# Optimization experiments

Measured on AMD Instinct MI355X. Metric: run time of the kernel, lower is better.

Reference implementation:

```python
import jax, jax.numpy as jnp
import numpy as np
import math

OUT_H, OUT_W = 608 // 4, 1088 // 4   # 152, 272
HW = OUT_H * OUT_W                   # 41344
MAX_OBJS = 256
N_ANN = 64
NID = 537
EMB_DIM = 256
EMB_SCALE = math.sqrt(2.0) * math.log(NID - 1.0)
B = 8


def gaussian_radius(height, width, min_overlap=0.7):
    # standard CenterNet radius; height/width are jnp.ceil'd box sizes
    b1 = height + width
    c1 = width * height * (1.0 - min_overlap) / (1.0 + min_overlap)
    r1 = (b1 + jnp.sqrt(jnp.maximum(b1 * b1 - 4.0 * c1, 0.0))) / 2.0
    b2 = 2.0 * (height + width)
    c2 = (1.0 - min_overlap) * width * height
    r2 = (b2 + jnp.sqrt(jnp.maximum(b2 * b2 - 16.0 * c2, 0.0))) / 2.0
    b3 = -2.0 * min_overlap * (height + width)
    c3 = (min_overlap - 1.0) * width * height
    r3 = (b3 + jnp.sqrt(jnp.maximum(b3 * b3 - 16.0 * min_overlap * c3, 0.0))) / 2.0
    return jnp.minimum(jnp.minimum(r1, r2), r3)


def build_targets(ann1, ann2):
    # ann cols: [cx, cy, w, h, cls, pid, vis, extra]; boxes normalized to [0,1]
    cx_raw = ann1[:, 0] * OUT_W
    cy_raw = ann1[:, 1] * OUT_H
    w = ann1[:, 2] * OUT_W
    h = ann1[:, 3] * OUT_H
    # amodal box from UNclipped center (torch deepcopies before clipping)
    x1 = cx_raw - 0.5 * w; y1 = cy_raw - 0.5 * h
    x2 = x1 + w;           y2 = y1 + h
    cx = jnp.clip(cx_raw, 0.0, OUT_W - 1.0)
    cy = jnp.clip(cy_raw, 0.0, OUT_H - 1.0)
    ctx = cx.astype(jnp.int32)
    cty = cy.astype(jnp.int32)
    radius = jnp.maximum(jnp.floor(gaussian_radius(jnp.ceil(h), jnp.ceil(w))), 0.0)

    # batched gaussian splat, max-reduced over objects (draw_umich_gaussian)
    sigma = (2.0 * radius + 1.0) / 6.0
    dx = jnp.arange(OUT_W, dtype=jnp.float32)[None, :] - ctx[:, None].astype(jnp.float32)  # [N,W]
    dy = jnp.arange(OUT_H, dtype=jnp.float32)[None, :] - cty[:, None].astype(jnp.float32)  # [N,H]
    g = jnp.exp(-(dy[:, :, None] ** 2 + dx[:, None, :] ** 2) / (2.0 * sigma[:, None, None] ** 2))  # [N,H,W]
    win = (jnp.abs(dy)[:, :, None] <= radius[:, None, None]) & (jnp.abs(dx)[:, None, :] <= radius[:, None, None])
    hm = jnp.max(jnp.where(win, g, 0.0), axis=0)  # [H,W]

    # first match of each object's pid in the next frame (torch breaks at first hit)
    pid1 = ann1[:, 5]
    match = pid1[:, None] == ann2[None, :, 5]
    has = match.any(axis=1)
    t1 = ann2[jnp.argmax(match, axis=1)]
    cx2 = t1[:, 0] * OUT_W; cy2 = t1[:, 1] * OUT_H
    w2 = t1[:, 2] * OUT_W;  h2 = t1[:, 3] * OUT_H
    x1t = cx2 - 0.5 * w2; y1t = cy2 - 0.5 * h2
    x2t = x1t + w2;       y2t = y1t + h2

    valid = has & (h > 0) & (w > 0) & (h2 > 0) & (w2 > 0)
    vm = valid.astype(jnp.float32)
    cxf = ctx.astype(jnp.float32); cyf = cty.astype(jnp.float32)
    wh = jnp.stack([cxf - x1, x2 - cxf, cyf - y1, y2 - cyf,
                    cxf - x1t, x2t - cxf, cyf - y1t, y2t - cyf], axis=-1) * vm[:, None]
    ind = jnp.where(valid, cty * OUT_W + ctx, 0)
    v = ann1[:, 6] * vm
    ids = jnp.where(valid, pid1.astype(jnp.int32), 0)

    pad = MAX_OBJS - N_ANN
    return (hm,
            jnp.pad(ind, (0, pad)),
            jnp.pad(vm, (0, pad)),
            jnp.pad(wh, ((0, pad), (0, 0))),
            jnp.pad(v, (0, pad)),
            jnp.pad(ids, (0, pad)))


def focal_loss(pred, gt):
    # CenterNet focal loss; pred already sigmoid+clamped
    pos = (gt == 1.0).astype(pred.dtype)
    pos_loss = (jnp.log(pred) * (1.0 - pred) ** 2 * pos).sum()
    neg_loss = (jnp.log(1.0 - pred) * pred ** 2 * (1.0 - gt) ** 4 * (1.0 - pos)).sum()
    num_pos = pos.sum()
    return jnp.where(num_pos > 0, -(pos_loss + neg_loss) / jnp.maximum(num_pos, 1.0), -neg_loss)


def reg_loss(feat, mask, ind, target):
    # feat [C,HW]; gather per-object channels, masked smooth-L1 sum / num_valid
    pred = feat[:, ind].T                       # [max_objs, C]
    m = mask[:, None]
    d = jnp.abs(pred * m - target * m)
    sl1 = jnp.where(d < 1.0, 0.5 * d * d, d - 0.5)
    return sl1.sum() / (mask.sum() + 1e-4)


def id_loss(identi, ind, mask, v, ids, W_id, b_id):
    feat = identi[:, ind].T                     # [max_objs, 256]
    feat = EMB_SCALE * feat / jnp.maximum(jnp.linalg.norm(feat, axis=-1, keepdims=True), 1e-12)
    logits = feat @ W_id.T + b_id               # [max_objs, 537]
    logp = jax.nn.log_softmax(logits, axis=-1)
    nll = -v * jnp.take_along_axis(logp, ids[:, None], axis=1)[:, 0]
    return (nll * mask).sum() / jnp.maximum(mask.sum(), 1.0)


def reference(classifications, regressions, viss, identis, annotations1, annotations2, W_id, b_id, s_det, s_id):
    cls = jnp.clip(jax.nn.sigmoid(classifications), 1e-4, 1.0 - 1e-4)   # [B,1,HW]
    vis = jnp.clip(jax.nn.sigmoid(viss), 1e-4, 1.0 - 1e-4)              # [B,1,HW]
    hm, ind, mask, wh, v, ids = jax.vmap(build_targets)(annotations1, annotations2)
    cls_l = jax.vmap(lambda p, g: focal_loss(p.reshape(OUT_H, OUT_W), g))(cls, hm)
    reg_l = jax.vmap(reg_loss)(regressions, mask, ind, wh)
    vis_l = jax.vmap(lambda f, m, i, t: reg_loss(f, m, i, t[:, None]))(vis, mask, ind, v)
    id_l = jax.vmap(lambda f, i, m, vv, ii: id_loss(f, i, m, vv, ii, W_id, b_id))(identis, ind, mask, v, ids)
    return (cls_l.mean(keepdims=True), reg_l.mean(keepdims=True), vis_l.mean(keepdims=True),
            id_l.mean(keepdims=True), s_det, s_id)


def setup_inputs() -> dict:
    key = jax.random.key(0)
    ks = jax.random.split(key, 8)
    classifications = jax.random.normal(ks[0], (B, 1, HW), dtype=jnp.float32)
    regressions = jax.random.normal(ks[1], (B, 8, HW), dtype=jnp.float32)
    viss = jax.random.normal(ks[2], (B, 1, HW), dtype=jnp.float32)
    identis = jax.random.normal(ks[3], (B, EMB_DIM, HW), dtype=jnp.float32)

    def make_frame_pair(k):
        k1, k2, k3, k4, k5, k6, k7 = jax.random.split(k, 7)
        cx = jax.random.uniform(k1, (N_ANN,), minval=0.05, maxval=0.95)
        cy = jax.random.uniform(k2, (N_ANN,), minval=0.05, maxval=0.95)
        w = jax.random.uniform(k3, (N_ANN,), minval=0.02, maxval=0.25)
        h = jax.random.uniform(k4, (N_ANN,), minval=0.05, maxval=0.4)
        pid = jax.random.permutation(k5, NID)[:N_ANN].astype(jnp.float32)  # unique track ids
        vis = jax.random.uniform(k6, (N_ANN,))
        extra = jax.random.uniform(k7, (N_ANN,))
        cls = jnp.zeros((N_ANN,), dtype=jnp.float32)
        a1 = jnp.stack([cx, cy, w, h, cls, pid, vis, extra], axis=-1)
        kp, kj = jax.random.split(jax.random.fold_in(k, 99))
        a2 = a1[jax.random.permutation(kp, N_ANN)]
        a2 = a2.at[:, 0:2].add(0.01 * jax.random.normal(kj, (N_ANN, 2)))
        a2 = a2.at[:, 0:2].set(jnp.clip(a2[:, 0:2], 0.05, 0.95))
        return a1, a2

    pairs = [make_frame_pair(jax.random.fold_in(ks[4], b)) for b in range(B)]
    annotations1 = jnp.stack([p[0] for p in pairs])
    annotations2 = jnp.stack([p[1] for p in pairs])
    W_id = 0.02 * jax.random.normal(ks[5], (NID, EMB_DIM), dtype=jnp.float32)
    b_id = jnp.zeros((NID,), dtype=jnp.float32)
    s_det = jnp.array([-1.85], dtype=jnp.float32)
    s_id = jnp.array([-1.05], dtype=jnp.float32)
    return {"classifications": classifications, "regressions": regressions, "viss": viss,
            "identis": identis, "annotations1": annotations1, "annotations2": annotations2,
            "W_id": W_id, "b_id": b_id, "s_det": s_det, "s_id": s_id}
```

## Files before the change

kernel.cpp:

```cpp
#include <hip/hip_runtime.h>
#include <math.h>

#define OUT_H 152
#define OUT_W 272
#define HW 41344
#define NOBJ 64
#define NB 8
#define NID 537
#define EMB 256

#define NFBLK 162
#define NFOCAL (NFBLK * NB)
#define NIDBLK (NB * NOBJ)

#define OF_FP    0
#define OF_IDNLL (NFOCAL * 3)

__device__ inline float waveRedSum(float v) {
  for (int off = 32; off; off >>= 1) v += __shfl_down(v, off, 64);
  return v;
}
__device__ inline float waveRedMax(float v) {
  for (int off = 32; off; off >>= 1) v = fmaxf(v, __shfl_down(v, off, 64));
  return v;
}

struct PrepOut {
  float cxf, cyf, radius, inv2s2, vm, v;
  float wh[8];
  int ind, id;
};

__device__ __forceinline__ PrepOut prep_obj(const float* __restrict__ ann1,
                                            const float* __restrict__ ann2,
                                            int b, int i) {
  const float* a1 = ann1 + (b * NOBJ + i) * 8;
  const float* A2 = ann2 + b * NOBJ * 8;

  float cx_raw = a1[0] * (float)OUT_W;
  float cy_raw = a1[1] * (float)OUT_H;
  float w = a1[2] * (float)OUT_W;
  float h = a1[3] * (float)OUT_H;
  float x1 = cx_raw - 0.5f * w, y1 = cy_raw - 0.5f * h;
  float x2 = x1 + w, y2 = y1 + h;
  float cx = fminf(fmaxf(cx_raw, 0.f), (float)(OUT_W - 1));
  float cy = fminf(fmaxf(cy_raw, 0.f), (float)(OUT_H - 1));
  int ctx = (int)cx, cty = (int)cy;

  float hc = ceilf(h), wc = ceilf(w);
  float b1 = hc + wc;
  float c1 = wc * hc * 0.3f / 1.7f;
  float r1 = (b1 + sqrtf(fmaxf(b1 * b1 - 4.f * c1, 0.f))) * 0.5f;
  float b2 = 2.f * (hc + wc);
  float c2 = 0.3f * wc * hc;
  float r2 = (b2 + sqrtf(fmaxf(b2 * b2 - 16.f * c2, 0.f))) * 0.5f;
  float b3 = -1.4f * (hc + wc);
  float c3 = -0.3f * wc * hc;
  float r3 = (b3 + sqrtf(fmaxf(b3 * b3 - 11.2f * c3, 0.f))) * 0.5f;
  float radius = fmaxf(floorf(fminf(fminf(r1, r2), r3)), 0.f);
  float sigma = (2.f * radius + 1.f) / 6.f;

  PrepOut P;
  P.cxf = (float)ctx;
  P.cyf = (float)cty;
  P.radius = radius;
  P.inv2s2 = 1.f / (2.f * sigma * sigma);

  float pid = a1[5];
  int jm = -1;
  for (int j = 0; j < NOBJ; ++j) {
    if (A2[j * 8 + 5] == pid) { jm = j; break; }
  }
  bool has = (jm >= 0);
  const float* t1 = A2 + (has ? jm : 0) * 8;
  float cx2 = t1[0] * (float)OUT_W, cy2 = t1[1] * (float)OUT_H;
  float w2 = t1[2] * (float)OUT_W, h2 = t1[3] * (float)OUT_H;
  float x1t = cx2 - 0.5f * w2, y1t = cy2 - 0.5f * h2;
  float x2t = x1t + w2, y2t = y1t + h2;

  bool valid = has && (h > 0.f) && (w > 0.f) && (h2 > 0.f) && (w2 > 0.f);
  float vm = valid ? 1.f : 0.f;
  P.vm = vm;
  P.v = a1[6] * vm;
  P.wh[0] = (P.cxf - x1) * vm;  P.wh[1] = (x2 - P.cxf) * vm;
  P.wh[2] = (P.cyf - y1) * vm;  P.wh[3] = (y2 - P.cyf) * vm;
  P.wh[4] = (P.cxf - x1t) * vm; P.wh[5] = (x2t - P.cxf) * vm;
  P.wh[6] = (P.cyf - y1t) * vm; P.wh[7] = (y2t - P.cyf) * vm;
  P.ind = valid ? (cty * OUT_W + ctx) : 0;
  P.id = valid ? (int)pid : 0;
  return P;
}

__global__ void __launch_bounds__(256)
main_kernel(const float* __restrict__ cls,
            const float* __restrict__ identis,
            const float* __restrict__ W_id,
            const float* __restrict__ b_id,
            const float* __restrict__ ann1,
            const float* __restrict__ ann2,
            float* __restrict__ F) {
  if (blockIdx.x < NFOCAL) {
    int blk = blockIdx.x;
    int b = blk / NFBLK;
    int bx = blk - b * NFBLK;
    int p = bx * 256 + threadIdx.x;

    __shared__ float s_ctx[64], s_cty[64], s_rad[64], s_inv[64];
    if (threadIdx.x < 64) {
      PrepOut P = prep_obj(ann1, ann2, b, threadIdx.x);
      s_ctx[threadIdx.x] = P.cxf;
      s_cty[threadIdx.x] = P.cyf;
      s_rad[threadIdx.x] = P.radius;
      s_inv[threadIdx.x] = P.inv2s2;
    }
    __syncthreads();

    float pos_l = 0.f, neg_l = 0.f, npos = 0.f;
    if (p < HW) {
      float xf = (float)(p % OUT_W);
      float yf = (float)(p / OUT_W);
      float gt = 0.f;
      #pragma unroll 8
      for (int o = 0; o < 64; ++o) {
        float dy = yf - s_cty[o];
        float dx = xf - s_ctx[o];
        float r = s_rad[o];
        if (fabsf(dy) <= r && fabsf(dx) <= r) {
          gt = fmaxf(gt, expf(-(dy * dy + dx * dx) * s_inv[o]));
        }
      }
      float x = cls[b * HW + p];
      float pr = 1.f / (1.f + expf(-x));
      pr = fminf(fmaxf(pr, 1e-4f), 0.9999f);
      if (gt == 1.f) {
        float om = 1.f - pr;
        pos_l = logf(pr) * om * om;
        npos = 1.f;
      } else {
        float omg = 1.f - gt;
        float w4 = omg * omg;
        w4 *= w4;
        neg_l = logf(1.f - pr) * pr * pr * w4;
      }
    }

    __shared__ float red[3][4];
    int wid = threadIdx.x >> 6, lane = threadIdx.x & 63;
    float a = waveRedSum(pos_l);
    float c = waveRedSum(neg_l);
    float n = waveRedSum(npos);
    if (lane == 0) { red[0][wid] = a; red[1][wid] = c; red[2][wid] = n; }
    __syncthreads();
    if (threadIdx.x == 0) {
      float pa = 0.f, pc = 0.f, pn = 0.f;
      for (int k = 0; k < 4; ++k) { pa += red[0][k]; pc += red[1][k]; pn += red[2][k]; }
      F[OF_FP + blk * 3 + 0] = pa;
      F[OF_FP + blk * 3 + 1] = pc;
      F[OF_FP + blk * 3 + 2] = pn;
    }
  } else {
    int o = blockIdx.x - NFOCAL;
    int b = o >> 6, i = o & 63;
    PrepOut P = prep_obj(ann1, ann2, b, i);
    if (P.vm == 0.f) {
      if (threadIdx.x == 0) F[OF_IDNLL + o] = 0.f;
      return;
    }
    int t = threadIdx.x;
    __shared__ float shf[EMB];
    __shared__ float slog[544];
    __shared__ float red4[4];
    int wid = t >> 6, lane = t & 63;

    float f = identis[(size_t)b * EMB * HW + (size_t)t * HW + P.ind];
    float n2 = waveRedSum(f * f);
    if (lane == 0) red4[wid] = n2;
    __syncthreads();
    float norm2 = red4[0] + red4[1] + red4[2] + red4[3];
    const float EMB_SCALE = 1.41421356237309515f * logf(536.0f);
    float scale = EMB_SCALE / fmaxf(sqrtf(norm2), 1e-12f);
    shf[t] = f * scale;
    __syncthreads();

    for (int c = t; c < NID; c += 256) {
      float acc = b_id[c];
      const float* wr = W_id + (size_t)c * EMB;
      #pragma unroll 4
      for (int k = 0; k < EMB; k += 4) {
        acc += shf[k] * wr[k] + shf[k + 1] * wr[k + 1] +
               shf[k + 2] * wr[k + 2] + shf[k + 3] * wr[k + 3];
      }
      slog[c] = acc;
    }
    __syncthreads();

    float mx = -1e30f;
    for (int c = t; c < NID; c += 256) mx = fmaxf(mx, slog[c]);
    mx = waveRedMax(mx);
    __syncthreads();
    if (lane == 0) red4[wid] = mx;
    __syncthreads();
    mx = fmaxf(fmaxf(red4[0], red4[1]), fmaxf(red4[2], red4[3]));

    float se = 0.f;
    for (int c = t; c < NID; c += 256) se += expf(slog[c] - mx);
    se = waveRedSum(se);
    __syncthreads();
    if (lane == 0) red4[wid] = se;
    __syncthreads();

    if (t == 0) {
      float sesum = red4[0] + red4[1] + red4[2] + red4[3];
      float lse = mx + logf(sesum);
      F[OF_IDNLL + o] = -P.v * (slog[P.id] - lse);
    }
  }
}

__global__ void __launch_bounds__(512)
final_kernel(const float* __restrict__ reg,
             const float* __restrict__ viss,
             const float* __restrict__ ann1,
             const float* __restrict__ ann2,
             const float* __restrict__ F,
             const float* __restrict__ s_det,
             const float* __restrict__ s_id,
             float* __restrict__ out) {
  int t = threadIdx.x;
  int b = t >> 6;
  int lane = t & 63;

  PrepOut P = prep_obj(ann1, ann2, b, lane);
  float msum = waveRedSum(P.vm);

  float rsum = 0.f, vsum = 0.f;
  if (P.vm > 0.f) {
    for (int c = 0; c < 8; ++c) {
      float pred = reg[(b * 8 + c) * HW + P.ind];
      float d = fabsf(pred - P.wh[c]);
      rsum += (d < 1.f) ? 0.5f * d * d : d - 0.5f;
    }
    float s = 1.f / (1.f + expf(-viss[b * HW + P.ind]));
    s = fminf(fmaxf(s, 1e-4f), 0.9999f);
    float d = fabsf(s - P.v);
    vsum += (d < 1.f) ? 0.5f * d * d : d - 0.5f;
  }
  rsum = waveRedSum(rsum);
  vsum = waveRedSum(vsum);

  float pa = 0.f, pc = 0.f, pn = 0.f;
  for (int e = lane; e < NFBLK; e += 64) {
    const float* fp = F + OF_FP + (b * NFBLK + e) * 3;
    pa += fp[0]; pc += fp[1]; pn += fp[2];
  }
  pa = waveRedSum(pa);
  pc = waveRedSum(pc);
  pn = waveRedSum(pn);

  float idv = waveRedSum(F[OF_IDNLL + b * 64 + lane]);

  __shared__ float L[8][4];
  if (lane == 0) {
    L[b][0] = (pn > 0.f) ? (-(pa + pc) / fmaxf(pn, 1.f)) : (-pc);
    L[b][1] = rsum / (msum + 0.0001f);
    L[b][2] = vsum / (msum + 0.0001f);
    L[b][3] = idv / fmaxf(msum, 1.f);
  }
  __syncthreads();
  if (t == 0) {
    float cl = 0.f, rl = 0.f, vl = 0.f, il = 0.f;
    for (int k = 0; k < 8; ++k) {
      cl += L[k][0]; rl += L[k][1]; vl += L[k][2]; il += L[k][3];
    }
    out[0] = cl / 8.f;
    out[1] = rl / 8.f;
    out[2] = vl / 8.f;
    out[3] = il / 8.f;
    out[4] = s_det[0];
    out[5] = s_id[0];
  }
}

extern "C" void kernel_launch(void* const* d_in, const int* in_sizes, int n_in,
                              void* d_out, int out_size, void* d_ws, size_t ws_size,
                              hipStream_t stream) {
  const float* cls     = (const float*)d_in[0];
  const float* reg     = (const float*)d_in[1];
  const float* viss    = (const float*)d_in[2];
  const float* identis = (const float*)d_in[3];
  const float* ann1    = (const float*)d_in[4];
  const float* ann2    = (const float*)d_in[5];
  const float* W_id    = (const float*)d_in[6];
  const float* b_id    = (const float*)d_in[7];
  const float* s_det   = (const float*)d_in[8];
  const float* s_id    = (const float*)d_in[9];
  float* F = (float*)d_ws;

  main_kernel<<<NFOCAL + NIDBLK, 256, 0, stream>>>(cls, identis, W_id, b_id,
                                                   ann1, ann2, F);
  final_kernel<<<1, 512, 0, stream>>>(reg, viss, ann1, ann2, F,
                                      s_det, s_id, (float*)d_out);
}
```

Before: 60.58 us.

## Move reg/vis loss into ID blocks and use wave-cooperative coalesced logits GEMV

The per-object regression and visibility smooth-L1 terms move out of the single-block final kernel into the per-object ID blocks. They are written as partial sums to the workspace, so the serial tail kernel only reduces precomputed values. The ID logits loop changes from one thread per class reading a whole weight row with strided access to one wave per group of four rows. Each lane loads a float4 of the row, and the partial dot products are combined with shuffle reductions, giving coalesced weight reads. The cost is more shuffle work and lane-0-only stores of the logits.

```diff
diff --git a/kernel.cpp b/kernel.cpp
--- a/kernel.cpp
+++ b/kernel.cpp
@@ -15,6 +15,9 @@
 
 #define OF_FP    0
 #define OF_IDNLL (NFOCAL * 3)
+#define OF_REGP  (OF_IDNLL + 512)
+#define OF_VISP  (OF_REGP + 512)
+#define OF_VMV   (OF_VISP + 512)
 
 __device__ inline float waveRedSum(float v) {
   for (int off = 32; off; off >>= 1) v += __shfl_down(v, off, 64);
@@ -93,6 +96,8 @@
 
 __global__ void __launch_bounds__(256)
 main_kernel(const float* __restrict__ cls,
+            const float* __restrict__ reg,
+            const float* __restrict__ viss,
             const float* __restrict__ identis,
             const float* __restrict__ W_id,
             const float* __restrict__ b_id,
@@ -161,16 +166,39 @@
   } else {
     int o = blockIdx.x - NFOCAL;
     int b = o >> 6, i = o & 63;
+    int t = threadIdx.x;
+    int wid = t >> 6, lane = t & 63;
     PrepOut P = prep_obj(ann1, ann2, b, i);
+
+    if (wid == 0) {
+      float rv = 0.f, vv = 0.f;
+      if (lane < 8) {
+        float pred = reg[(b * 8 + lane) * HW + P.ind];
+        float d = fabsf(pred * P.vm - P.wh[lane]);
+        rv = (d < 1.f) ? 0.5f * d * d : d - 0.5f;
+      } else if (lane == 8) {
+        float s = 1.f / (1.f + expf(-viss[b * HW + P.ind]));
+        s = fminf(fmaxf(s, 1e-4f), 0.9999f);
+        float d = fabsf(s * P.vm - P.v);
+        vv = (d < 1.f) ? 0.5f * d * d : d - 0.5f;
+      }
+      rv = waveRedSum(rv);
+      vv = waveRedSum(vv);
+      if (lane == 0) {
+        F[OF_REGP + o] = rv;
+        F[OF_VISP + o] = vv;
+        F[OF_VMV + o]  = P.vm;
+      }
+    }
+
     if (P.vm == 0.f) {
-      if (threadIdx.x == 0) F[OF_IDNLL + o] = 0.f;
+      if (t == 0) F[OF_IDNLL + o] = 0.f;
       return;
     }
-    int t = threadIdx.x;
+
     __shared__ float shf[EMB];
     __shared__ float slog[544];
     __shared__ float red4[4];
-    int wid = t >> 6, lane = t & 63;
 
     float f = identis[(size_t)b * EMB * HW + (size_t)t * HW + P.ind];
     float n2 = waveRedSum(f * f);
@@ -182,15 +210,30 @@
     shf[t] = f * scale;
     __syncthreads();
 
-    for (int c = t; c < NID; c += 256) {
-      float acc = b_id[c];
-      const float* wr = W_id + (size_t)c * EMB;
-      #pragma unroll 4
-      for (int k = 0; k < EMB; k += 4) {
-        acc += shf[k] * wr[k] + shf[k + 1] * wr[k + 1] +
-               shf[k + 2] * wr[k + 2] + shf[k + 3] * wr[k + 3];
-      }
-      slog[c] = acc;
+    float4 s4 = *(const float4*)&shf[lane * 4];
+    for (int r0 = wid * 4; r0 < NID; r0 += 16) {
+      float acc[4];
+      #pragma unroll
+      for (int rr = 0; rr < 4; ++rr) {
+        int r = r0 + rr;
+        float ax = 0.f;
+        if (r < NID) {
+          const float4 wv = *(const float4*)&W_id[(size_t)r * EMB + lane * 4];
+          ax = wv.x * s4.x + wv.y * s4.y + wv.z * s4.z + wv.w * s4.w;
+        }
+        acc[rr] = ax;
+      }
+      #pragma unroll
+      for (int rr = 0; rr < 4; ++rr)
+        for (int off = 32; off; off >>= 1)
+          acc[rr] += __shfl_down(acc[rr], off, 64);
+      if (lane == 0) {
+        #pragma unroll
+        for (int rr = 0; rr < 4; ++rr) {
+          int r = r0 + rr;
+          if (r < NID) slog[r] = acc[rr] + b_id[r];
+        }
+      }
     }
     __syncthreads();
 
@@ -218,11 +261,7 @@
 }
 
 __global__ void __launch_bounds__(512)
-final_kernel(const float* __restrict__ reg,
-             const float* __restrict__ viss,
-             const float* __restrict__ ann1,
-             const float* __restrict__ ann2,
-             const float* __restrict__ F,
+final_kernel(const float* __restrict__ F,
              const float* __restrict__ s_det,
              const float* __restrict__ s_id,
              float* __restrict__ out) {
@@ -230,24 +269,6 @@
   int b = t >> 6;
   int lane = t & 63;
 
-  PrepOut P = prep_obj(ann1, ann2, b, lane);
-  float msum = waveRedSum(P.vm);
-
-  float rsum = 0.f, vsum = 0.f;
-  if (P.vm > 0.f) {
-    for (int c = 0; c < 8; ++c) {
-      float pred = reg[(b * 8 + c) * HW + P.ind];
-      float d = fabsf(pred - P.wh[c]);
-      rsum += (d < 1.f) ? 0.5f * d * d : d - 0.5f;
-    }
-    float s = 1.f / (1.f + expf(-viss[b * HW + P.ind]));
-    s = fminf(fmaxf(s, 1e-4f), 0.9999f);
-    float d = fabsf(s - P.v);
-    vsum += (d < 1.f) ? 0.5f * d * d : d - 0.5f;
-  }
-  rsum = waveRedSum(rsum);
-  vsum = waveRedSum(vsum);
-
   float pa = 0.f, pc = 0.f, pn = 0.f;
   for (int e = lane; e < NFBLK; e += 64) {
     const float* fp = F + OF_FP + (b * NFBLK + e) * 3;
@@ -257,7 +278,10 @@
   pc = waveRedSum(pc);
   pn = waveRedSum(pn);
 
-  float idv = waveRedSum(F[OF_IDNLL + b * 64 + lane]);
+  float rsum = waveRedSum(F[OF_REGP + b * 64 + lane]);
+  float vsum = waveRedSum(F[OF_VISP + b * 64 + lane]);
+  float msum = waveRedSum(F[OF_VMV  + b * 64 + lane]);
+  float idv  = waveRedSum(F[OF_IDNLL + b * 64 + lane]);
 
   __shared__ float L[8][4];
   if (lane == 0) {
@@ -296,8 +320,7 @@
   const float* s_id    = (const float*)d_in[9];
   float* F = (float*)d_ws;
 
-  main_kernel<<<NFOCAL + NIDBLK, 256, 0, stream>>>(cls, identis, W_id, b_id,
-                                                   ann1, ann2, F);
-  final_kernel<<<1, 512, 0, stream>>>(reg, viss, ann1, ann2, F,
-                                      s_det, s_id, (float*)d_out);
-}
+  main_kernel<<<NFOCAL + NIDBLK, 256, 0, stream>>>(cls, reg, viss, identis,
+                                                   W_id, b_id, ann1, ann2, F);
+  final_kernel<<<1, 512, 0, stream>>>(F, s_det, s_id, (float*)d_out);
+}
```

New measurement: 69.48 us. 1.15x slower.

## Cull gaussian objects per block via ballot mask, use fast math, vectorize ID GEMV

Applied to the files above, without the earlier changes.

Each focal block now computes a 64-bit ballot mask of the objects whose gaussian window overlaps the block's pixel rows or columns, and iterates only over those objects. Object centers and radii are packed into one integer per object. Precise exp and log are replaced with __expf and __logf throughout, and the ID-classifier dot product uses float4 loads. This cuts per-pixel loop work and transcendental cost, at the price of slightly lower math precision and a dependence on the integer bit-packing ranges.

```diff
diff --git a/kernel.cpp b/kernel.cpp
--- a/kernel.cpp
+++ b/kernel.cpp
@@ -103,15 +103,26 @@
     int blk = blockIdx.x;
     int b = blk / NFBLK;
     int bx = blk - b * NFBLK;
-    int p = bx * 256 + threadIdx.x;
-
-    __shared__ float s_ctx[64], s_cty[64], s_rad[64], s_inv[64];
+    int p0 = bx * 256;
+    int p = p0 + threadIdx.x;
+
+    __shared__ unsigned s_pk[64];
+    __shared__ float s_inv[64];
+    __shared__ unsigned long long s_mask;
     if (threadIdx.x < 64) {
       PrepOut P = prep_obj(ann1, ann2, b, threadIdx.x);
-      s_ctx[threadIdx.x] = P.cxf;
-      s_cty[threadIdx.x] = P.cyf;
-      s_rad[threadIdx.x] = P.radius;
+      int ctx = (int)P.cxf, cty = (int)P.cyf, r = (int)P.radius;
+      s_pk[threadIdx.x]  = (unsigned)ctx | ((unsigned)cty << 9) | ((unsigned)r << 17);
       s_inv[threadIdx.x] = P.inv2s2;
+      int y0 = p0 / OUT_W;
+      int y1 = (p0 + 255) / OUT_W;
+      bool two_rows = (y1 > y0);
+      int x0 = two_rows ? 0 : (p0 - y0 * OUT_W);
+      int x1 = two_rows ? (OUT_W - 1) : (p0 + 255 - y0 * OUT_W);
+      bool act = (cty + r >= y0) && (cty - r <= y1) &&
+                 (ctx + r >= x0) && (ctx - r <= x1);
+      unsigned long long m = __ballot(act);
+      if (threadIdx.x == 0) s_mask = m;
     }
     __syncthreads();
 
@@ -120,27 +131,33 @@
       float xf = (float)(p % OUT_W);
       float yf = (float)(p / OUT_W);
       float gt = 0.f;
-      #pragma unroll 8
-      for (int o = 0; o < 64; ++o) {
-        float dy = yf - s_cty[o];
-        float dx = xf - s_ctx[o];
-        float r = s_rad[o];
-        if (fabsf(dy) <= r && fabsf(dx) <= r) {
-          gt = fmaxf(gt, expf(-(dy * dy + dx * dx) * s_inv[o]));
+      unsigned long long m = s_mask;
+      while (m) {
+        int o = __ffsll((unsigned long long)m) - 1;
+        m &= m - 1;
+        unsigned pk = s_pk[o];
+        float inv = s_inv[o];
+        float cxv = (float)(pk & 511u);
+        float cyv = (float)((pk >> 9) & 255u);
+        float rv  = (float)(pk >> 17);
+        float dy = yf - cyv;
+        float dx = xf - cxv;
+        if (fabsf(dy) <= rv && fabsf(dx) <= rv) {
+          gt = fmaxf(gt, __expf(-(dy * dy + dx * dx) * inv));
         }
       }
       float x = cls[b * HW + p];
-      float pr = 1.f / (1.f + expf(-x));
+      float pr = 1.f / (1.f + __expf(-x));
       pr = fminf(fmaxf(pr, 1e-4f), 0.9999f);
       if (gt == 1.f) {
         float om = 1.f - pr;
-        pos_l = logf(pr) * om * om;
+        pos_l = __logf(pr) * om * om;
         npos = 1.f;
       } else {
         float omg = 1.f - gt;
         float w4 = omg * omg;
         w4 *= w4;
-        neg_l = logf(1.f - pr) * pr * pr * w4;
+        neg_l = __logf(1.f - pr) * pr * pr * w4;
       }
     }
 
@@ -185,10 +202,11 @@
     for (int c = t; c < NID; c += 256) {
       float acc = b_id[c];
       const float* wr = W_id + (size_t)c * EMB;
-      #pragma unroll 4
+      #pragma unroll 8
       for (int k = 0; k < EMB; k += 4) {
-        acc += shf[k] * wr[k] + shf[k + 1] * wr[k + 1] +
-               shf[k + 2] * wr[k + 2] + shf[k + 3] * wr[k + 3];
+        float4 wv = *(const float4*)(wr + k);
+        float4 sv = *(const float4*)(&shf[k]);
+        acc += wv.x * sv.x + wv.y * sv.y + wv.z * sv.z + wv.w * sv.w;
       }
       slog[c] = acc;
     }
@@ -203,7 +221,7 @@
     mx = fmaxf(fmaxf(red4[0], red4[1]), fmaxf(red4[2], red4[3]));
 
     float se = 0.f;
-    for (int c = t; c < NID; c += 256) se += expf(slog[c] - mx);
+    for (int c = t; c < NID; c += 256) se += __expf(slog[c] - mx);
     se = waveRedSum(se);
     __syncthreads();
     if (lane == 0) red4[wid] = se;
@@ -211,7 +229,7 @@
 
     if (t == 0) {
       float sesum = red4[0] + red4[1] + red4[2] + red4[3];
-      float lse = mx + logf(sesum);
+      float lse = mx + __logf(sesum);
       F[OF_IDNLL + o] = -P.v * (slog[P.id] - lse);
     }
   }
@@ -240,7 +258,7 @@
       float d = fabsf(pred - P.wh[c]);
       rsum += (d < 1.f) ? 0.5f * d * d : d - 0.5f;
     }
-    float s = 1.f / (1.f + expf(-viss[b * HW + P.ind]));
+    float s = 1.f / (1.f + __expf(-viss[b * HW + P.ind]));
     s = fminf(fmaxf(s, 1e-4f), 0.9999f);
     float d = fabsf(s - P.v);
     vsum += (d < 1.f) ? 0.5f * d * d : d - 0.5f;
```

New measurement: 60.91 us. Within noise of the previous version (+0.5%).
